# Kernel tuning notes

Hardware: AMD Instinct MI355X
Metric: run time of the kernel (lower is better)

The kernel has to match this reference:

```python
import jax, jax.numpy as jnp
import numpy as np

K = 1024          # num_embeddings
D = 256           # embedding_dim
COMMIT = 0.1      # commitment_cost
EPS = float(np.finfo(np.float32).eps)


def setup_inputs() -> dict:
    key = jax.random.key(0)
    k1, k2 = jax.random.split(key)
    X = jax.random.normal(k1, (16, 4096, D), dtype=jnp.float32)
    # matches nn.Embedding init: uniform(-1/K, 1/K)
    emb_weight = jax.random.uniform(k2, (K, D), dtype=jnp.float32,
                                    minval=-1.0 / K, maxval=1.0 / K)
    return {"X": X, "emb_weight": emb_weight}


def reference(X, emb_weight):
    B, N, Dm = X.shape
    Xf = X.reshape(-1, Dm)                                  # [BN, D]
    dist = (jnp.sum(Xf * Xf, axis=-1, keepdims=True)
            + jnp.sum(emb_weight * emb_weight, axis=-1)
            - 2.0 * Xf @ emb_weight.T)                      # [BN, K]
    idx = jnp.argmin(dist, axis=-1)                         # [BN]
    # one-hot @ codebook == gather
    quantized = emb_weight[idx].reshape(X.shape)            # [B, N, D]
    # perplexity from one-hot mean == normalized counts
    counts = jnp.zeros((K,), dtype=X.dtype).at[idx].add(1.0)
    avg_probs = counts / Xf.shape[0]
    perplexity = jnp.exp(-jnp.sum(avg_probs * jnp.log(avg_probs + EPS)))
    # vq loss (learnable codebook branch)
    sg = jax.lax.stop_gradient
    e_latent = jnp.mean((sg(quantized) - X) ** 2)
    q_latent = jnp.mean((quantized - sg(X)) ** 2)
    loss_vq = q_latent + COMMIT * e_latent
    # straight-through estimator
    quantized_st = X + sg(quantized - X)
    encoding_indices = idx.reshape(B, N)
    return quantized_st, encoding_indices, perplexity, loss_vq
```

## Files before the change

### kernel.cpp

```cpp
#include <hip/hip_runtime.h>
#include <math.h>

#define ROWS 65536
#define DIM  256
#define KC   1024
#define NQ   (ROWS * DIM)


__device__ __forceinline__ float sq_sum_numpy(const float* __restrict__ p) {
    float halves[2];
#pragma unroll
    for (int h = 0; h < 2; ++h) {
        const float* a = p + h * 128;
        float4 u0 = *(const float4*)(a);
        float4 u1 = *(const float4*)(a + 4);
        float r0 = __fmul_rn(u0.x, u0.x);
        float r1 = __fmul_rn(u0.y, u0.y);
        float r2 = __fmul_rn(u0.z, u0.z);
        float r3 = __fmul_rn(u0.w, u0.w);
        float r4 = __fmul_rn(u1.x, u1.x);
        float r5 = __fmul_rn(u1.y, u1.y);
        float r6 = __fmul_rn(u1.z, u1.z);
        float r7 = __fmul_rn(u1.w, u1.w);
        for (int i = 8; i < 128; i += 8) {
            float4 v0 = *(const float4*)(a + i);
            float4 v1 = *(const float4*)(a + i + 4);
            r0 = __fadd_rn(r0, __fmul_rn(v0.x, v0.x));
            r1 = __fadd_rn(r1, __fmul_rn(v0.y, v0.y));
            r2 = __fadd_rn(r2, __fmul_rn(v0.z, v0.z));
            r3 = __fadd_rn(r3, __fmul_rn(v0.w, v0.w));
            r4 = __fadd_rn(r4, __fmul_rn(v1.x, v1.x));
            r5 = __fadd_rn(r5, __fmul_rn(v1.y, v1.y));
            r6 = __fadd_rn(r6, __fmul_rn(v1.z, v1.z));
            r7 = __fadd_rn(r7, __fmul_rn(v1.w, v1.w));
        }
        float s01 = __fadd_rn(r0, r1);
        float s23 = __fadd_rn(r2, r3);
        float s45 = __fadd_rn(r4, r5);
        float s67 = __fadd_rn(r6, r7);
        halves[h] = __fadd_rn(__fadd_rn(s01, s23), __fadd_rn(s45, s67));
    }
    return __fadd_rn(halves[0], halves[1]);
}

__global__ __launch_bounds__(256) void k_prepB(const float* __restrict__ E,
                                               float* __restrict__ B32) {
    int j = blockIdx.x * 256 + threadIdx.x;
    if (j >= KC) return;
    B32[j] = sq_sum_numpy(E + (size_t)j * DIM);
}

__global__ __launch_bounds__(256) void k_prepA(const float* __restrict__ X,
                                               float* __restrict__ Arr) {
    int r = blockIdx.x * 256 + threadIdx.x;
    Arr[r] = sq_sum_numpy(X + (size_t)r * DIM);
}

#define TM 128
#define TN 128
#define TD 32
#define LSTR 132

__global__ __launch_bounds__(256) void k_pass1(
    const float* __restrict__ X, const float* __restrict__ E,
    const float* __restrict__ B32, const float* __restrict__ Arr,
    int* __restrict__ idx32)
{
    __shared__ float sm[2 * TD * LSTR];
    float* Xs = sm;
    float* Es = sm + TD * LSTR;

    const int tid = threadIdx.x;
    const int tx = tid & 15;
    const int ty = tid >> 4;
    const int rowbase = blockIdx.x * TM;

    float a8[8];
#pragma unroll
    for (int i = 0; i < 8; ++i) a8[i] = Arr[rowbase + ty * 8 + i];

    float v1[8]; int i1[8];
#pragma unroll
    for (int i = 0; i < 8; ++i) { v1[i] = 3.0e38f; i1[i] = 0; }

    for (int cb = 0; cb < KC; cb += TN) {
        float acc[8][8];
#pragma unroll
        for (int i = 0; i < 8; ++i)
#pragma unroll
            for (int j = 0; j < 8; ++j) acc[i][j] = 0.0f;

        for (int dc = 0; dc < DIM; dc += TD) {
            __syncthreads();
#pragma unroll
            for (int k = 0; k < 4; ++k) {
                int fi  = tid + k * 256;
                int r   = fi >> 3;
                int dd4 = (fi & 7) * 4;
                float4 xv = *(const float4*)(X + (size_t)(rowbase + r) * DIM + dc + dd4);
                Xs[(dd4 + 0) * LSTR + r] = xv.x;
                Xs[(dd4 + 1) * LSTR + r] = xv.y;
                Xs[(dd4 + 2) * LSTR + r] = xv.z;
                Xs[(dd4 + 3) * LSTR + r] = xv.w;
                float4 ev = *(const float4*)(E + (size_t)(cb + r) * DIM + dc + dd4);
                Es[(dd4 + 0) * LSTR + r] = ev.x;
                Es[(dd4 + 1) * LSTR + r] = ev.y;
                Es[(dd4 + 2) * LSTR + r] = ev.z;
                Es[(dd4 + 3) * LSTR + r] = ev.w;
            }
            __syncthreads();

#pragma unroll 8
            for (int dd = 0; dd < TD; ++dd) {
                float xr[8], er[8];
                float4 t0 = *(float4*)&Xs[dd * LSTR + ty * 8];
                float4 t1 = *(float4*)&Xs[dd * LSTR + ty * 8 + 4];
                xr[0]=t0.x; xr[1]=t0.y; xr[2]=t0.z; xr[3]=t0.w;
                xr[4]=t1.x; xr[5]=t1.y; xr[6]=t1.z; xr[7]=t1.w;
                float4 u0 = *(float4*)&Es[dd * LSTR + tx * 8];
                float4 u1 = *(float4*)&Es[dd * LSTR + tx * 8 + 4];
                er[0]=u0.x; er[1]=u0.y; er[2]=u0.z; er[3]=u0.w;
                er[4]=u1.x; er[5]=u1.y; er[6]=u1.z; er[7]=u1.w;
#pragma unroll
                for (int i = 0; i < 8; ++i)
#pragma unroll
                    for (int j = 0; j < 8; ++j)
                        acc[i][j] = fmaf(xr[i], er[j], acc[i][j]);
            }
        }

#pragma unroll
        for (int j = 0; j < 8; ++j) {
            int c = cb + tx * 8 + j;
            float b = B32[c];
#pragma unroll
            for (int i = 0; i < 8; ++i) {
                float Cv = __fmul_rn(2.0f, acc[i][j]);
                float t1v = __fadd_rn(a8[i], b);
                float dv  = __fsub_rn(t1v, Cv);
                if (dv < v1[i]) { v1[i] = dv; i1[i] = c; }
            }
        }
    }

    __syncthreads();
    float* Mv = sm;
    int*   Mi = (int*)(sm + 2048);
#pragma unroll
    for (int i = 0; i < 8; ++i) {
        int r = ty * 8 + i;
        Mv[r * 16 + tx] = v1[i];
        Mi[r * 16 + tx] = i1[i];
    }
    __syncthreads();
    if (tid < TM) {
        int r = tid;
        float bv = Mv[r * 16];
        int   bi = Mi[r * 16];
        for (int t = 1; t < 16; ++t) {
            float av = Mv[r * 16 + t];
            int   ai = Mi[r * 16 + t];
            if (av < bv || (av == bv && ai < bi)) { bv = av; bi = ai; }
        }
        idx32[rowbase + r] = bi;
    }
}

__global__ __launch_bounds__(256) void k_out(
    const float* __restrict__ X, const float* __restrict__ E,
    const int* __restrict__ idx32, float* __restrict__ out0,
    double* __restrict__ lossacc)
{
    const int NF4 = NQ / 4;
    double s = 0.0;
    for (int g = blockIdx.x * blockDim.x + threadIdx.x; g < NF4;
         g += gridDim.x * blockDim.x) {
        int row = g >> 6;
        int d4  = g & 63;
        int j = idx32[row];
        float4 q = *(const float4*)(E + (size_t)j * DIM + d4 * 4);
        float4 x = *(const float4*)(X + (size_t)g * 4);
        *(float4*)(out0 + (size_t)g * 4) = q;
        double dx;
        dx = (double)q.x - (double)x.x; s = fma(dx, dx, s);
        dx = (double)q.y - (double)x.y; s = fma(dx, dx, s);
        dx = (double)q.z - (double)x.z; s = fma(dx, dx, s);
        dx = (double)q.w - (double)x.w; s = fma(dx, dx, s);
    }
#pragma unroll
    for (int off = 32; off > 0; off >>= 1) s += __shfl_down(s, off, 64);
    __shared__ double wsum[4];
    int lane = threadIdx.x & 63, wv = threadIdx.x >> 6;
    if (lane == 0) wsum[wv] = s;
    __syncthreads();
    if (threadIdx.x == 0) {
        double t = wsum[0] + wsum[1] + wsum[2] + wsum[3];
        atomicAdd(lossacc, t);
    }
}

__global__ __launch_bounds__(256) void k_idxout(
    const int* __restrict__ idx32, float* __restrict__ out1,
    int* __restrict__ counts)
{
    __shared__ int h[KC];
    for (int i = threadIdx.x; i < KC; i += 256) h[i] = 0;
    __syncthreads();
    int r = blockIdx.x * 256 + threadIdx.x;
    int j = idx32[r];
    out1[r] = (float)j;
    atomicAdd(&h[j], 1);
    __syncthreads();
    for (int i = threadIdx.x; i < KC; i += 256)
        if (h[i]) atomicAdd(&counts[i], h[i]);
}

__global__ void k_fin(const int* __restrict__ counts,
                      const double* __restrict__ lossacc,
                      float* __restrict__ out_pl)
{
    __shared__ double sh[256];
    double s = 0.0;
    for (int i = threadIdx.x; i < KC; i += 256) {
        double p = (double)counts[i] / 65536.0;
        s += p * log(p + 1.1920928955078125e-07);
    }
    sh[threadIdx.x] = s;
    __syncthreads();
    for (int off = 128; off > 0; off >>= 1) {
        if (threadIdx.x < off) sh[threadIdx.x] += sh[threadIdx.x + off];
        __syncthreads();
    }
    if (threadIdx.x == 0) {
        out_pl[0] = (float)exp(-sh[0]);
        out_pl[1] = (float)((*lossacc / (double)NQ) * 1.1);
    }
}

extern "C" void kernel_launch(void* const* d_in, const int* in_sizes, int n_in,
                              void* d_out, int out_size, void* d_ws, size_t ws_size,
                              hipStream_t stream) {
    const float* X = (const float*)d_in[0];
    const float* E = (const float*)d_in[1];
    float* out = (float*)d_out;
    char* ws = (char*)d_ws;

    double* lossacc = (double*)(ws + 0);
    int*    counts  = (int*)(ws + 16);
    float*  B32     = (float*)(ws + 4224);
    float*  Arr     = (float*)(ws + 8320);
    int*    idx32   = (int*)(ws + 270464);

    hipMemsetAsync(d_ws, 0, 4224, stream);

    hipLaunchKernelGGL(k_prepB, dim3(4),        dim3(256), 0, stream, E, B32);
    hipLaunchKernelGGL(k_prepA, dim3(256),      dim3(256), 0, stream, X, Arr);
    hipLaunchKernelGGL(k_pass1, dim3(ROWS / TM), dim3(256), 0, stream,
                       X, E, B32, Arr, idx32);
    hipLaunchKernelGGL(k_out,   dim3(2048),     dim3(256), 0, stream,
                       X, E, idx32, out, lossacc);
    hipLaunchKernelGGL(k_idxout, dim3(256),     dim3(256), 0, stream,
                       idx32, out + NQ, counts);
    hipLaunchKernelGGL(k_fin,   dim3(1),        dim3(256), 0, stream,
                       counts, lossacc, out + NQ + 65536);
}
```

Baseline: 606.6 us.

## Split codebook across blocks and merge argmin via packed 64-bit atomicMin

The distance/argmin kernel now splits the 1024 codebook entries over two blocks in a second grid dimension, doubling the number of blocks to better fill the GPU. Partial minima are merged with a 64-bit atomicMin on packed (distance bits, index), which relies on distances being non-negative. Shared tiles switch to a row-major layout with float4 stores and strided row ownership per thread, and launch bounds request higher occupancy. In exchange, X tiles are loaded twice and an extra 512 KB memset is needed to initialise the packed buffer.

```diff
diff --git a/kernel.cpp b/kernel.cpp
--- a/kernel.cpp
+++ b/kernel.cpp
@@ -59,31 +59,32 @@
 #define TM 128
 #define TN 128
 #define TD 32
-#define LSTR 132
-
-__global__ __launch_bounds__(256) void k_pass1(
+#define STR 36
+
+__global__ __launch_bounds__(256, 4) void k_pass1(
     const float* __restrict__ X, const float* __restrict__ E,
     const float* __restrict__ B32, const float* __restrict__ Arr,
-    int* __restrict__ idx32)
-{
-    __shared__ float sm[2 * TD * LSTR];
+    unsigned long long* __restrict__ packed)
+{
+    __shared__ float sm[2 * TM * STR];
     float* Xs = sm;
-    float* Es = sm + TD * LSTR;
+    float* Es = sm + TM * STR;
 
     const int tid = threadIdx.x;
     const int tx = tid & 15;
     const int ty = tid >> 4;
     const int rowbase = blockIdx.x * TM;
+    const int colbase = blockIdx.y * 512;
 
     float a8[8];
 #pragma unroll
-    for (int i = 0; i < 8; ++i) a8[i] = Arr[rowbase + ty * 8 + i];
+    for (int i = 0; i < 8; ++i) a8[i] = Arr[rowbase + ty + 16 * i];
 
     float v1[8]; int i1[8];
 #pragma unroll
     for (int i = 0; i < 8; ++i) { v1[i] = 3.0e38f; i1[i] = 0; }
 
-    for (int cb = 0; cb < KC; cb += TN) {
+    for (int cb = 0; cb < 512; cb += TN) {
         float acc[8][8];
 #pragma unroll
         for (int i = 0; i < 8; ++i)
@@ -94,48 +95,43 @@
             __syncthreads();
 #pragma unroll
             for (int k = 0; k < 4; ++k) {
-                int fi  = tid + k * 256;
-                int r   = fi >> 3;
-                int dd4 = (fi & 7) * 4;
-                float4 xv = *(const float4*)(X + (size_t)(rowbase + r) * DIM + dc + dd4);
-                Xs[(dd4 + 0) * LSTR + r] = xv.x;
-                Xs[(dd4 + 1) * LSTR + r] = xv.y;
-                Xs[(dd4 + 2) * LSTR + r] = xv.z;
-                Xs[(dd4 + 3) * LSTR + r] = xv.w;
-                float4 ev = *(const float4*)(E + (size_t)(cb + r) * DIM + dc + dd4);
-                Es[(dd4 + 0) * LSTR + r] = ev.x;
-                Es[(dd4 + 1) * LSTR + r] = ev.y;
-                Es[(dd4 + 2) * LSTR + r] = ev.z;
-                Es[(dd4 + 3) * LSTR + r] = ev.w;
+                int fi = tid + k * 256;
+                int r  = fi >> 3;
+                int g4 = (fi & 7) * 4;
+                float4 xv = *(const float4*)(X + (size_t)(rowbase + r) * DIM + dc + g4);
+                *(float4*)&Xs[r * STR + g4] = xv;
+                float4 ev = *(const float4*)(E + (size_t)(colbase + cb + r) * DIM + dc + g4);
+                *(float4*)&Es[r * STR + g4] = ev;
             }
             __syncthreads();
 
-#pragma unroll 8
-            for (int dd = 0; dd < TD; ++dd) {
-                float xr[8], er[8];
-                float4 t0 = *(float4*)&Xs[dd * LSTR + ty * 8];
-                float4 t1 = *(float4*)&Xs[dd * LSTR + ty * 8 + 4];
-                xr[0]=t0.x; xr[1]=t0.y; xr[2]=t0.z; xr[3]=t0.w;
-                xr[4]=t1.x; xr[5]=t1.y; xr[6]=t1.z; xr[7]=t1.w;
-                float4 u0 = *(float4*)&Es[dd * LSTR + tx * 8];
-                float4 u1 = *(float4*)&Es[dd * LSTR + tx * 8 + 4];
-                er[0]=u0.x; er[1]=u0.y; er[2]=u0.z; er[3]=u0.w;
-                er[4]=u1.x; er[5]=u1.y; er[6]=u1.z; er[7]=u1.w;
-#pragma unroll
-                for (int i = 0; i < 8; ++i)
-#pragma unroll
-                    for (int j = 0; j < 8; ++j)
-                        acc[i][j] = fmaf(xr[i], er[j], acc[i][j]);
+#pragma unroll
+            for (int gg = 0; gg < 8; ++gg) {
+                float4 e4[8];
+#pragma unroll
+                for (int j = 0; j < 8; ++j)
+                    e4[j] = *(float4*)&Es[(tx + 16 * j) * STR + gg * 4];
+#pragma unroll
+                for (int i = 0; i < 8; ++i) {
+                    float4 x4 = *(float4*)&Xs[(ty + 16 * i) * STR + gg * 4];
+#pragma unroll
+                    for (int j = 0; j < 8; ++j) {
+                        acc[i][j] = fmaf(x4.x, e4[j].x, acc[i][j]);
+                        acc[i][j] = fmaf(x4.y, e4[j].y, acc[i][j]);
+                        acc[i][j] = fmaf(x4.z, e4[j].z, acc[i][j]);
+                        acc[i][j] = fmaf(x4.w, e4[j].w, acc[i][j]);
+                    }
+                }
             }
         }
 
 #pragma unroll
         for (int j = 0; j < 8; ++j) {
-            int c = cb + tx * 8 + j;
+            int c = colbase + cb + tx + 16 * j;
             float b = B32[c];
 #pragma unroll
             for (int i = 0; i < 8; ++i) {
-                float Cv = __fmul_rn(2.0f, acc[i][j]);
+                float Cv  = __fmul_rn(2.0f, acc[i][j]);
                 float t1v = __fadd_rn(a8[i], b);
                 float dv  = __fsub_rn(t1v, Cv);
                 if (dv < v1[i]) { v1[i] = dv; i1[i] = c; }
@@ -148,7 +144,7 @@
     int*   Mi = (int*)(sm + 2048);
 #pragma unroll
     for (int i = 0; i < 8; ++i) {
-        int r = ty * 8 + i;
+        int r = ty + 16 * i;
         Mv[r * 16 + tx] = v1[i];
         Mi[r * 16 + tx] = i1[i];
     }
@@ -162,13 +158,16 @@
             int   ai = Mi[r * 16 + t];
             if (av < bv || (av == bv && ai < bi)) { bv = av; bi = ai; }
         }
-        idx32[rowbase + r] = bi;
+        unsigned long long pk =
+            ((unsigned long long)__float_as_uint(bv) << 32) |
+            (unsigned long long)(unsigned)bi;
+        atomicMin(&packed[rowbase + r], pk);
     }
 }
 
 __global__ __launch_bounds__(256) void k_out(
     const float* __restrict__ X, const float* __restrict__ E,
-    const int* __restrict__ idx32, float* __restrict__ out0,
+    const unsigned long long* __restrict__ packed, float* __restrict__ out0,
     double* __restrict__ lossacc)
 {
     const int NF4 = NQ / 4;
@@ -177,7 +176,7 @@
          g += gridDim.x * blockDim.x) {
         int row = g >> 6;
         int d4  = g & 63;
-        int j = idx32[row];
+        int j = (int)(packed[row] & 0xffffffffULL);
         float4 q = *(const float4*)(E + (size_t)j * DIM + d4 * 4);
         float4 x = *(const float4*)(X + (size_t)g * 4);
         *(float4*)(out0 + (size_t)g * 4) = q;
@@ -200,14 +199,14 @@
 }
 
 __global__ __launch_bounds__(256) void k_idxout(
-    const int* __restrict__ idx32, float* __restrict__ out1,
+    const unsigned long long* __restrict__ packed, float* __restrict__ out1,
     int* __restrict__ counts)
 {
     __shared__ int h[KC];
     for (int i = threadIdx.x; i < KC; i += 256) h[i] = 0;
     __syncthreads();
     int r = blockIdx.x * 256 + threadIdx.x;
-    int j = idx32[r];
+    int j = (int)(packed[r] & 0xffffffffULL);
     out1[r] = (float)j;
     atomicAdd(&h[j], 1);
     __syncthreads();
@@ -249,18 +248,19 @@
     int*    counts  = (int*)(ws + 16);
     float*  B32     = (float*)(ws + 4224);
     float*  Arr     = (float*)(ws + 8320);
-    int*    idx32   = (int*)(ws + 270464);
-
-    hipMemsetAsync(d_ws, 0, 4224, stream);
-
-    hipLaunchKernelGGL(k_prepB, dim3(4),        dim3(256), 0, stream, E, B32);
-    hipLaunchKernelGGL(k_prepA, dim3(256),      dim3(256), 0, stream, X, Arr);
-    hipLaunchKernelGGL(k_pass1, dim3(ROWS / TM), dim3(256), 0, stream,
-                       X, E, B32, Arr, idx32);
-    hipLaunchKernelGGL(k_out,   dim3(2048),     dim3(256), 0, stream,
-                       X, E, idx32, out, lossacc);
-    hipLaunchKernelGGL(k_idxout, dim3(256),     dim3(256), 0, stream,
-                       idx32, out + NQ, counts);
-    hipLaunchKernelGGL(k_fin,   dim3(1),        dim3(256), 0, stream,
+    unsigned long long* packed = (unsigned long long*)(ws + 270464);
+
+    hipMemsetAsync(ws, 0, 4224, stream);
+    hipMemsetAsync(ws + 270464, 0xFF, 524288, stream);
+
+    hipLaunchKernelGGL(k_prepB, dim3(4),   dim3(256), 0, stream, E, B32);
+    hipLaunchKernelGGL(k_prepA, dim3(256), dim3(256), 0, stream, X, Arr);
+    hipLaunchKernelGGL(k_pass1, dim3(ROWS / TM, 2), dim3(256), 0, stream,
+                       X, E, B32, Arr, packed);
+    hipLaunchKernelGGL(k_out,   dim3(2048), dim3(256), 0, stream,
+                       X, E, packed, out, lossacc);
+    hipLaunchKernelGGL(k_idxout, dim3(256), dim3(256), 0, stream,
+                       packed, out + NQ, counts);
+    hipLaunchKernelGGL(k_fin,   dim3(1),   dim3(256), 0, stream,
                        counts, lossacc, out + NQ + 65536);
 }
```

Measured after the change: 694.9 us. 14.6% more time.
